# Kernel tuning notes

Hardware: AMD Instinct MI355X
Metric: run time of the kernel (lower is better)

Reference implementation:

```python
import jax, jax.numpy as jnp
import numpy as np

B, S, D, H = 4, 2048, 1024, 16
HD = D // H  # head dim = 64


def setup_inputs() -> dict:
    key = jax.random.key(0)
    ks = jax.random.split(key, 12)
    s = 1.0 / np.sqrt(D)
    return {
        "query": jax.random.normal(ks[0], (B, S, D), jnp.float32),
        "key": jax.random.normal(ks[1], (B, S, D), jnp.float32),
        "value": jax.random.normal(ks[2], (B, S, D), jnp.float32),
        "attention_mask": jnp.zeros((B, S, S), jnp.float32),
        "Wq": jax.random.normal(ks[3], (D, D), jnp.float32) * s,
        "bq": jax.random.normal(ks[4], (D,), jnp.float32) * s,
        "Wk": jax.random.normal(ks[5], (D, D), jnp.float32) * s,
        "bk": jax.random.normal(ks[6], (D,), jnp.float32) * s,
        "Wv": jax.random.normal(ks[7], (D, D), jnp.float32) * s,
        "bv": jax.random.normal(ks[8], (D,), jnp.float32) * s,
        "Wo": jax.random.normal(ks[9], (D, D), jnp.float32) * s,
        "bo": jax.random.normal(ks[10], (D,), jnp.float32) * s,
    }


def reference(query, key, value, attention_mask, Wq, bq, Wk, bk, Wv, bv, Wo, bo):
    # projections (torch Linear: x @ W.T + b)
    q = query @ Wq.T + bq
    k = key @ Wk.T + bk
    v = value @ Wv.T + bv
    # split heads: [B, S, D] -> [B, H, S, HD]
    split = lambda x: x.reshape(B, S, H, HD).transpose(0, 2, 1, 3)
    q, k, v = split(q), split(k), split(v)
    # scores: [B, H, Sq, Sk], scaled and masked (mask broadcast over heads)
    scores = jnp.einsum("bhqd,bhkd->bhqk", q, k) / jnp.sqrt(jnp.asarray(HD, q.dtype))
    scores = scores + attention_mask[:, None, :, :]
    probs = jax.nn.softmax(scores, axis=-1)
    out = jnp.einsum("bhqk,bhkd->bhqd", probs, v)
    # concat heads: [B, H, S, HD] -> [B, S, D]
    out = out.transpose(0, 2, 1, 3).reshape(B, S, D)
    return out @ Wo.T + bo
```

## Files before the change

kernel.cpp:

```cpp
#include <hip/hip_runtime.h>
#include <hip/hip_bf16.h>


typedef float f32x4 __attribute__((ext_vector_type(4)));
typedef float f32x16 __attribute__((ext_vector_type(16)));
typedef short bf16x8 __attribute__((ext_vector_type(8)));

#define LOG2E 1.4426950408889634f

__device__ __forceinline__ void gload_lds16(const void* g, void* l) {
  __builtin_amdgcn_global_load_lds((const __attribute__((address_space(1))) void*)g,
                                   (__attribute__((address_space(3))) void*)l,
                                   16, 0, 0);
}

__device__ __forceinline__ float fast_exp2(float x) {
#if __has_builtin(__builtin_amdgcn_exp2f)
  return __builtin_amdgcn_exp2f(x);
#else
  return exp2f(x);
#endif
}

__device__ __forceinline__ unsigned cvt_pk_bf16(float a, float b) {
  unsigned r;
  asm("v_cvt_pk_bf16_f32 %0, %1, %2" : "=v"(r) : "v"(a), "v"(b));
  return r;
}

__device__ __forceinline__ void pl32swap(unsigned& a, unsigned& b, int hi) {
#if __has_builtin(__builtin_amdgcn_permlane32_swap)
  typedef unsigned uint2v __attribute__((ext_vector_type(2)));
  uint2v r = __builtin_amdgcn_permlane32_swap(a, b, false, false);
  a = r[0];
  b = r[1];
#else
  unsigned ax = __shfl_xor((int)a, 32);
  unsigned bx = __shfl_xor((int)b, 32);
  unsigned na = hi ? bx : a;
  unsigned nb = hi ? b : ax;
  a = na;
  b = nb;
#endif
}

__device__ __forceinline__ bf16x8 lds_read_swz(const __hip_bfloat16* base, int row, int colByte) {
  int off = row * 128 + (colByte ^ ((row & 7) << 4));
  return *(const bf16x8*)((const char*)base + off);
}

__global__ __launch_bounds__(256) void cvt3(const float* __restrict__ s0,
                                            const float* __restrict__ s1,
                                            const float* __restrict__ s2,
                                            __hip_bfloat16* __restrict__ d0,
                                            __hip_bfloat16* __restrict__ d1,
                                            __hip_bfloat16* __restrict__ d2, int n) {
  const float* s = blockIdx.z == 0 ? s0 : (blockIdx.z == 1 ? s1 : s2);
  __hip_bfloat16* d = blockIdx.z == 0 ? d0 : (blockIdx.z == 1 ? d1 : d2);
  int i = (blockIdx.x * 256 + threadIdx.x) * 8;
  if (i + 8 <= n) {
    float4 x = *(const float4*)(s + i);
    float4 y = *(const float4*)(s + i + 4);
    bf16x8 v;
    __hip_bfloat16* hv = (__hip_bfloat16*)&v;
    hv[0] = __float2bfloat16(x.x); hv[1] = __float2bfloat16(x.y);
    hv[2] = __float2bfloat16(x.z); hv[3] = __float2bfloat16(x.w);
    hv[4] = __float2bfloat16(y.x); hv[5] = __float2bfloat16(y.y);
    hv[6] = __float2bfloat16(y.z); hv[7] = __float2bfloat16(y.w);
    *(bf16x8*)(d + i) = v;
  }
}

__global__ __launch_bounds__(256) void cvt4(const float* __restrict__ s0,
                                            const float* __restrict__ s1,
                                            const float* __restrict__ s2,
                                            const float* __restrict__ s3,
                                            __hip_bfloat16* __restrict__ d0,
                                            __hip_bfloat16* __restrict__ d1,
                                            __hip_bfloat16* __restrict__ d2,
                                            __hip_bfloat16* __restrict__ d3, int n) {
  const float* s = blockIdx.z == 0 ? s0 : (blockIdx.z == 1 ? s1 : (blockIdx.z == 2 ? s2 : s3));
  __hip_bfloat16* d = blockIdx.z == 0 ? d0 : (blockIdx.z == 1 ? d1 : (blockIdx.z == 2 ? d2 : d3));
  int i = (blockIdx.x * 256 + threadIdx.x) * 8;
  if (i + 8 <= n) {
    float4 x = *(const float4*)(s + i);
    float4 y = *(const float4*)(s + i + 4);
    bf16x8 v;
    __hip_bfloat16* hv = (__hip_bfloat16*)&v;
    hv[0] = __float2bfloat16(x.x); hv[1] = __float2bfloat16(x.y);
    hv[2] = __float2bfloat16(x.z); hv[3] = __float2bfloat16(x.w);
    hv[4] = __float2bfloat16(y.x); hv[5] = __float2bfloat16(y.y);
    hv[6] = __float2bfloat16(y.z); hv[7] = __float2bfloat16(y.w);
    *(bf16x8*)(d + i) = v;
  }
}

__global__ __launch_bounds__(256) void maskrow(const float* __restrict__ m,
                                               unsigned char* __restrict__ flags) {
  int row = blockIdx.x * 4 + (threadIdx.x >> 6);
  int l = threadIdx.x & 63;
  const float* r = m + (size_t)row * 2048;
  float v0 = r[0];
  bool eq = true;
#pragma unroll
  for (int i = 0; i < 8; i++) {
    float4 x = *(const float4*)(r + l * 4 + i * 256);
    eq &= (x.x == v0) & (x.y == v0) & (x.z == v0) & (x.w == v0);
  }
  unsigned long long b = __ballot((int)eq);
  if (l == 0) flags[row] = (b == ~0ull) ? 1 : 0;
}

__device__ __forceinline__ void gemm_core(const __hip_bfloat16* __restrict__ A,
                                          const __hip_bfloat16* __restrict__ W,
                                          char* smem, int rowbase, int colbase,
                                          f32x4 acc[4][4]) {
  __hip_bfloat16(*As)[64] = (__hip_bfloat16(*)[64])smem;
  __hip_bfloat16(*Bs)[64] = (__hip_bfloat16(*)[64])(smem + 128 * 64 * 2);
  const int t = threadIdx.x;
  const int w = t >> 6, l = t & 63;
  const int wm = w >> 1, wn = w & 1;
  const int lr = l & 15, lg = l >> 4;
  const int srow = l >> 3, schunk = (l & 7) * 8;

#pragma unroll
  for (int m = 0; m < 4; m++)
#pragma unroll
    for (int n = 0; n < 4; n++) acc[m][n] = {0.f, 0.f, 0.f, 0.f};

  for (int kt = 0; kt < 16; ++kt) {
    const int k0 = kt * 64;
#pragma unroll
    for (int i = 0; i < 4; i++) {
      int r = w * 32 + i * 8;
      gload_lds16(A + (size_t)(rowbase + r + srow) * 1024 + k0 + schunk, &As[r][0]);
      gload_lds16(W + (size_t)(colbase + r + srow) * 1024 + k0 + schunk, &Bs[r][0]);
    }
    __syncthreads();
#pragma unroll
    for (int kk = 0; kk < 2; kk++) {
      bf16x8 a[4], b[4];
#pragma unroll
      for (int m = 0; m < 4; m++) a[m] = *(const bf16x8*)&As[wm * 64 + m * 16 + lr][kk * 32 + lg * 8];
#pragma unroll
      for (int n = 0; n < 4; n++) b[n] = *(const bf16x8*)&Bs[wn * 64 + n * 16 + lr][kk * 32 + lg * 8];
#pragma unroll
      for (int m = 0; m < 4; m++)
#pragma unroll
        for (int n = 0; n < 4; n++)
          acc[m][n] = __builtin_amdgcn_mfma_f32_16x16x32_bf16(a[m], b[n], acc[m][n], 0, 0, 0);
    }
    __syncthreads();
  }
}

template <int F32OUT>
__device__ __forceinline__ void gemm_store_rows(f32x4 acc[4][4], const float* __restrict__ bias,
                                                void* __restrict__ out, int rowbase, int colbase,
                                                float scale) {
  const int l = threadIdx.x & 63, w = threadIdx.x >> 6;
  const int wm = w >> 1, wn = w & 1;
  const int lr = l & 15, lg = l >> 4;
#pragma unroll
  for (int m = 0; m < 4; m++)
#pragma unroll
    for (int r = 0; r < 4; r++) {
      int gi = rowbase + wm * 64 + m * 16 + lg * 4 + r;
#pragma unroll
      for (int n = 0; n < 4; n++) {
        int gj = colbase + wn * 64 + n * 16 + lr;
        float v = (acc[m][n][r] + bias[gj]) * scale;
        if (F32OUT)
          ((float*)out)[(size_t)gi * 1024 + gj] = v;
        else
          ((__hip_bfloat16*)out)[(size_t)gi * 1024 + gj] = __float2bfloat16(v);
      }
    }
}

__device__ __forceinline__ void gemm_store_vT(f32x4 acc[4][4], const float* __restrict__ bias,
                                              __hip_bfloat16* __restrict__ out, char* smem,
                                              int rowbase, int colbase) {
  const int t = threadIdx.x, l = t & 63, w = t >> 6;
  const int wm = w >> 1, wn = w & 1;
  const int lr = l & 15, lg = l >> 4;
  __hip_bfloat16* Ts = (__hip_bfloat16*)smem;
#pragma unroll
  for (int m = 0; m < 4; m++)
#pragma unroll
    for (int r = 0; r < 4; r++) {
      int rr = wm * 64 + m * 16 + lg * 4 + r;
#pragma unroll
      for (int n = 0; n < 4; n++) {
        int c = wn * 64 + n * 16 + lr;
        Ts[rr * 130 + c] = __float2bfloat16(acc[m][n][r] + bias[colbase + c]);
      }
    }
  __syncthreads();
  int d = t >> 1, s0 = (t & 1) * 64;
  int gd = colbase + d;
  int h = gd >> 6, hd = gd & 63;
  int gs = rowbase + s0;
  int b = gs >> 11, sl = gs & 2047;
  __hip_bfloat16* dst = out + ((size_t)(b * 16 + h) * 64 + hd) * 2048 + sl;
#pragma unroll
  for (int c8 = 0; c8 < 8; c8++) {
    bf16x8 v;
#pragma unroll
    for (int j = 0; j < 8; j++)
      ((unsigned short*)&v)[j] = ((const unsigned short*)Ts)[(s0 + c8 * 8 + j) * 130 + d];
    *(bf16x8*)(dst + c8 * 8) = v;
  }
}

__global__ __launch_bounds__(256) void gemm_qkv(
    const __hip_bfloat16* __restrict__ vin, const __hip_bfloat16* __restrict__ kin,
    const __hip_bfloat16* __restrict__ qin, const __hip_bfloat16* __restrict__ wv,
    const __hip_bfloat16* __restrict__ wk, const __hip_bfloat16* __restrict__ wq,
    const float* __restrict__ bv, const float* __restrict__ bk, const float* __restrict__ bq,
    __hip_bfloat16* __restrict__ vT, __hip_bfloat16* __restrict__ kp,
    __hip_bfloat16* __restrict__ qp, float qscale) {
  extern __shared__ char smem[];
  const int z = blockIdx.z;
  const __hip_bfloat16* A = z == 0 ? vin : (z == 1 ? kin : qin);
  const __hip_bfloat16* W = z == 0 ? wv : (z == 1 ? wk : wq);
  const float* bias = z == 0 ? bv : (z == 1 ? bk : bq);
  const int rowbase = blockIdx.y * 128;
  const int colbase = blockIdx.x * 128;

  f32x4 acc[4][4];
  gemm_core(A, W, smem, rowbase, colbase, acc);

  if (z == 0) {
    gemm_store_vT(acc, bias, vT, smem, rowbase, colbase);
  } else {
    gemm_store_rows<0>(acc, bias, z == 1 ? (void*)kp : (void*)qp, rowbase, colbase,
                       z == 2 ? qscale : 1.0f);
  }
}

template <int MODE>
__global__ __launch_bounds__(256) void gemm_nt(const __hip_bfloat16* __restrict__ A,
                                               const __hip_bfloat16* __restrict__ W,
                                               const float* __restrict__ bias,
                                               void* __restrict__ out, float scale) {
  extern __shared__ char smem[];
  const int rowbase = blockIdx.y * 128;
  const int colbase = blockIdx.x * 128;
  f32x4 acc[4][4];
  gemm_core(A, W, smem, rowbase, colbase, acc);
  if (MODE == 1)
    gemm_store_vT(acc, bias, (__hip_bfloat16*)out, smem, rowbase, colbase);
  else if (MODE == 0)
    gemm_store_rows<0>(acc, bias, out, rowbase, colbase, scale);
  else
    gemm_store_rows<1>(acc, bias, out, rowbase, colbase, scale);
}

__global__ __launch_bounds__(256, 4) void attn(const __hip_bfloat16* __restrict__ Q,
                                               const __hip_bfloat16* __restrict__ K,
                                               const __hip_bfloat16* __restrict__ Vt,
                                               const float* __restrict__ mask,
                                               const unsigned char* __restrict__ flags,
                                               __hip_bfloat16* __restrict__ O) {
  __shared__ __hip_bfloat16 Ks[2][64][64];
  __shared__ __hip_bfloat16 Vs[2][64][64];

  const int t = threadIdx.x, w = t >> 6, l = t & 63;
  const int l31 = l & 31, hi = l >> 5;
  int lin = blockIdx.y * 16 + blockIdx.x;
  lin = (lin & 7) * 128 + (lin >> 3);
  const int qt = lin & 15, bh = lin >> 4;
  const int b = bh >> 4, h = bh & 15;
  const int q0 = qt * 128 + w * 32;
  const size_t bS = (size_t)b * 2048;
  const int srow = l >> 3;
  const int swchunk = ((l & 7) * 8) ^ (srow << 3);

#define STAGE(dbuf, ktile)                                                             \
  do {                                                                                 \
    int kb_ = (ktile) * 64;                                                            \
    _Pragma("unroll") for (int i_ = 0; i_ < 2; i_++) {                                 \
      int r_ = w * 16 + i_ * 8;                                                        \
      gload_lds16(K + (bS + kb_ + r_ + srow) * 1024 + h * 64 + swchunk,                \
                  &Ks[dbuf][r_][0]);                                                   \
      gload_lds16(Vt + ((size_t)bh * 64 + r_ + srow) * 2048 + kb_ + swchunk,           \
                  &Vs[dbuf][r_][0]);                                                   \
    }                                                                                  \
  } while (0)

  bf16x8 qf[4];
#pragma unroll
  for (int c = 0; c < 4; c++)
    qf[c] = *(const bf16x8*)(Q + (bS + q0 + l31) * 1024 + h * 64 + c * 16 + hi * 8);

  bf16x8 vones;
#pragma unroll
  for (int j = 0; j < 8; j++) ((unsigned short*)&vones)[j] = 0x3F80;

  f32x16 acco[2], psum;
#pragma unroll
  for (int i = 0; i < 16; i++) { acco[0][i] = 0.f; acco[1][i] = 0.f; psum[i] = 0.f; }
  float m2 = -1e30f;

  const bool need_mask = !__all((int)(flags[bS + q0 + l31] != 0));
  const float* mrowf = mask + (bS + q0 + l31) * 2048;

  STAGE(0, 0);
  __syncthreads();
  int cur = 0;

  for (int kt = 0; kt < 32; ++kt) {
    const int kb = kt * 64;
    if (kt < 31) STAGE(cur ^ 1, kt + 1);

    f32x16 sc[2];
    if (need_mask) {
#pragma unroll
      for (int ks = 0; ks < 2; ks++)
#pragma unroll
        for (int g = 0; g < 4; g++) {
          float4 tmp = *(const float4*)(mrowf + kb + ks * 32 + g * 8 + hi * 4);
          sc[ks][g * 4 + 0] = tmp.x * LOG2E; sc[ks][g * 4 + 1] = tmp.y * LOG2E;
          sc[ks][g * 4 + 2] = tmp.z * LOG2E; sc[ks][g * 4 + 3] = tmp.w * LOG2E;
        }
    } else {
#pragma unroll
      for (int i = 0; i < 16; i++) { sc[0][i] = 0.f; sc[1][i] = 0.f; }
    }

    __builtin_amdgcn_s_setprio(1);
#pragma unroll
    for (int c = 0; c < 4; c++) {
      bf16x8 ka0 = lds_read_swz(&Ks[cur][0][0], l31, c * 32 + hi * 16);
      sc[0] = __builtin_amdgcn_mfma_f32_32x32x16_bf16(ka0, qf[c], sc[0], 0, 0, 0);
      bf16x8 ka1 = lds_read_swz(&Ks[cur][0][0], 32 + l31, c * 32 + hi * 16);
      sc[1] = __builtin_amdgcn_mfma_f32_32x32x16_bf16(ka1, qf[c], sc[1], 0, 0, 0);
    }
    __builtin_amdgcn_s_setprio(0);

    float mx[16];
#pragma unroll
    for (int r = 0; r < 16; r++) mx[r] = fmaxf(sc[0][r], sc[1][r]);
#pragma unroll
    for (int s = 8; s >= 1; s >>= 1)
#pragma unroll
      for (int r = 0; r < s; r++) mx[r] = fmaxf(mx[r], mx[r + s]);
    float tmax = fmaxf(mx[0], __shfl_xor(mx[0], 32));

    if (__any(tmax > m2 + 8.0f)) {
      float mn = fmaxf(m2, tmax);
      float rs = fast_exp2(m2 - mn);
      m2 = mn;
#pragma unroll
      for (int r = 0; r < 16; r++) {
        float rsr = __shfl(rs, (r & 3) + 8 * (r >> 2) + 4 * hi);
        psum[r] *= rsr;
        acco[0][r] *= rsr;
        acco[1][r] *= rsr;
      }
    }

    unsigned pk[2][4][2];
#pragma unroll
    for (int ks = 0; ks < 2; ks++)
#pragma unroll
      for (int g = 0; g < 4; g++)
#pragma unroll
        for (int s = 0; s < 2; s++) {
          float p0 = fast_exp2(sc[ks][g * 4 + s * 2] - m2);
          float p1 = fast_exp2(sc[ks][g * 4 + s * 2 + 1] - m2);
          pk[ks][g][s] = cvt_pk_bf16(p0, p1);
        }

    __builtin_amdgcn_s_setprio(1);
#pragma unroll
    for (int ks = 0; ks < 2; ks++) {
#pragma unroll
      for (int c16 = 0; c16 < 2; c16++) {
        unsigned x0 = pk[ks][2 * c16][0], y0 = pk[ks][2 * c16 + 1][0];
        unsigned x1 = pk[ks][2 * c16][1], y1 = pk[ks][2 * c16 + 1][1];
        pl32swap(x0, y0, hi);
        pl32swap(x1, y1, hi);
        bf16x8 pa;
        ((unsigned*)&pa)[0] = x0; ((unsigned*)&pa)[1] = x1;
        ((unsigned*)&pa)[2] = y0; ((unsigned*)&pa)[3] = y1;
        psum = __builtin_amdgcn_mfma_f32_32x32x16_bf16(pa, vones, psum, 0, 0, 0);
#pragma unroll
        for (int ds = 0; ds < 2; ds++) {
          bf16x8 vb = lds_read_swz(&Vs[cur][0][0], ds * 32 + l31, ks * 64 + c16 * 32 + hi * 16);
          acco[ds] = __builtin_amdgcn_mfma_f32_32x32x16_bf16(pa, vb, acco[ds], 0, 0, 0);
        }
      }
    }
    __builtin_amdgcn_s_setprio(0);
    __syncthreads();
    cur ^= 1;
  }
#undef STAGE

#pragma unroll
  for (int r = 0; r < 16; r++) {
    float invr = 1.0f / psum[r];
    int q = q0 + (r & 3) + 8 * (r >> 2) + 4 * hi;
#pragma unroll
    for (int ds = 0; ds < 2; ds++)
      O[(bS + q) * 1024 + h * 64 + ds * 32 + l31] = __float2bfloat16(acco[ds][r] * invr);
  }
}

extern "C" void kernel_launch(void* const* d_in, const int* in_sizes, int n_in,
                              void* d_out, int out_size, void* d_ws, size_t ws_size,
                              hipStream_t stream) {
  const float* q = (const float*)d_in[0];
  const float* k = (const float*)d_in[1];
  const float* v = (const float*)d_in[2];
  const float* msk = (const float*)d_in[3];
  const float* Wq = (const float*)d_in[4];
  const float* bq = (const float*)d_in[5];
  const float* Wk = (const float*)d_in[6];
  const float* bk = (const float*)d_in[7];
  const float* Wv = (const float*)d_in[8];
  const float* bv = (const float*)d_in[9];
  const float* Wo = (const float*)d_in[10];
  const float* bo = (const float*)d_in[11];

  char* ws = (char*)d_ws;
  __hip_bfloat16* qin = (__hip_bfloat16*)(ws);
  __hip_bfloat16* kin = (__hip_bfloat16*)(ws + (16u << 20));
  __hip_bfloat16* vin = (__hip_bfloat16*)(ws + (32u << 20));
  __hip_bfloat16* wqb = (__hip_bfloat16*)(ws + (48u << 20));
  __hip_bfloat16* wkb = (__hip_bfloat16*)(ws + (50u << 20));
  __hip_bfloat16* wvb = (__hip_bfloat16*)(ws + (52u << 20));
  __hip_bfloat16* wob = (__hip_bfloat16*)(ws + (54u << 20));
  __hip_bfloat16* vT  = (__hip_bfloat16*)(ws + (56u << 20));

  const bool merged = ws_size >= (104ull << 20) + 8192;

  dim3 blk(256);
  size_t smem = 33280;
  const float qscale = 0.125f * LOG2E;

  cvt3<<<dim3(4096, 1, 3), blk, 0, stream>>>(q, k, v, qin, kin, vin, 8388608);
  cvt4<<<dim3(512, 1, 4), blk, 0, stream>>>(Wq, Wk, Wv, Wo, wqb, wkb, wvb, wob, 1048576);

  if (merged) {
    __hip_bfloat16* kp = (__hip_bfloat16*)(ws + (72u << 20));
    __hip_bfloat16* qp = (__hip_bfloat16*)(ws + (88u << 20));
    unsigned char* flags = (unsigned char*)(ws + (104u << 20));
    __hip_bfloat16* oat = qin;
    maskrow<<<dim3(2048), blk, 0, stream>>>(msk, flags);
    gemm_qkv<<<dim3(8, 64, 3), blk, smem, stream>>>(vin, kin, qin, wvb, wkb, wqb,
                                                    bv, bk, bq, vT, kp, qp, qscale);
    attn<<<dim3(16, 64), blk, 0, stream>>>(qp, kp, vT, msk, flags, oat);
    gemm_nt<2><<<dim3(8, 64), blk, smem, stream>>>(oat, wob, bo, (float*)d_out, 1.0f);
  } else {
    __hip_bfloat16* kp = vin;
    __hip_bfloat16* qp = kin;
    unsigned char* flags = (unsigned char*)(ws + (72u << 20));
    __hip_bfloat16* oat = qin;
    maskrow<<<dim3(2048), blk, 0, stream>>>(msk, flags);
    gemm_nt<1><<<dim3(8, 64), blk, smem, stream>>>(vin, wvb, bv, vT, 1.0f);
    gemm_nt<0><<<dim3(8, 64), blk, smem, stream>>>(kin, wkb, bk, kp, 1.0f);
    gemm_nt<0><<<dim3(8, 64), blk, smem, stream>>>(qin, wqb, bq, qp, qscale);
    attn<<<dim3(16, 64), blk, 0, stream>>>(qp, kp, vT, msk, flags, oat);
    gemm_nt<2><<<dim3(8, 64), blk, smem, stream>>>(oat, wob, bo, (float*)d_out, 1.0f);
  }
}
```

Measured before the change: 268.4 us.

## Fuse conversion and mask-check kernels; stage GEMM epilogue through LDS for coalesced stores

Merges the three preprocessing launches (activation cast, weight cast, mask-row uniformity check) into one kernel using blockIdx.z to select the work, so two launches and their gaps disappear. The GEMM row-store epilogue now writes accumulators into padded shared memory and then emits wide vector stores per row instead of scattered scalar stores. Shared memory per GEMM block grows slightly to hold the fp32 staging tile, and the fused kernel launches some idle blocks that return early.

```diff
diff --git a/kernel.cpp b/kernel.cpp
--- a/kernel.cpp
+++ b/kernel.cpp
@@ -49,66 +49,53 @@
   return *(const bf16x8*)((const char*)base + off);
 }
 
-__global__ __launch_bounds__(256) void cvt3(const float* __restrict__ s0,
-                                            const float* __restrict__ s1,
-                                            const float* __restrict__ s2,
-                                            __hip_bfloat16* __restrict__ d0,
-                                            __hip_bfloat16* __restrict__ d1,
-                                            __hip_bfloat16* __restrict__ d2, int n) {
-  const float* s = blockIdx.z == 0 ? s0 : (blockIdx.z == 1 ? s1 : s2);
-  __hip_bfloat16* d = blockIdx.z == 0 ? d0 : (blockIdx.z == 1 ? d1 : d2);
-  int i = (blockIdx.x * 256 + threadIdx.x) * 8;
-  if (i + 8 <= n) {
-    float4 x = *(const float4*)(s + i);
-    float4 y = *(const float4*)(s + i + 4);
-    bf16x8 v;
-    __hip_bfloat16* hv = (__hip_bfloat16*)&v;
-    hv[0] = __float2bfloat16(x.x); hv[1] = __float2bfloat16(x.y);
-    hv[2] = __float2bfloat16(x.z); hv[3] = __float2bfloat16(x.w);
-    hv[4] = __float2bfloat16(y.x); hv[5] = __float2bfloat16(y.y);
-    hv[6] = __float2bfloat16(y.z); hv[7] = __float2bfloat16(y.w);
-    *(bf16x8*)(d + i) = v;
-  }
-}
-
-__global__ __launch_bounds__(256) void cvt4(const float* __restrict__ s0,
-                                            const float* __restrict__ s1,
-                                            const float* __restrict__ s2,
-                                            const float* __restrict__ s3,
-                                            __hip_bfloat16* __restrict__ d0,
-                                            __hip_bfloat16* __restrict__ d1,
-                                            __hip_bfloat16* __restrict__ d2,
-                                            __hip_bfloat16* __restrict__ d3, int n) {
-  const float* s = blockIdx.z == 0 ? s0 : (blockIdx.z == 1 ? s1 : (blockIdx.z == 2 ? s2 : s3));
-  __hip_bfloat16* d = blockIdx.z == 0 ? d0 : (blockIdx.z == 1 ? d1 : (blockIdx.z == 2 ? d2 : d3));
-  int i = (blockIdx.x * 256 + threadIdx.x) * 8;
-  if (i + 8 <= n) {
-    float4 x = *(const float4*)(s + i);
-    float4 y = *(const float4*)(s + i + 4);
-    bf16x8 v;
-    __hip_bfloat16* hv = (__hip_bfloat16*)&v;
-    hv[0] = __float2bfloat16(x.x); hv[1] = __float2bfloat16(x.y);
-    hv[2] = __float2bfloat16(x.z); hv[3] = __float2bfloat16(x.w);
-    hv[4] = __float2bfloat16(y.x); hv[5] = __float2bfloat16(y.y);
-    hv[6] = __float2bfloat16(y.z); hv[7] = __float2bfloat16(y.w);
-    *(bf16x8*)(d + i) = v;
-  }
-}
-
-__global__ __launch_bounds__(256) void maskrow(const float* __restrict__ m,
-                                               unsigned char* __restrict__ flags) {
-  int row = blockIdx.x * 4 + (threadIdx.x >> 6);
-  int l = threadIdx.x & 63;
-  const float* r = m + (size_t)row * 2048;
-  float v0 = r[0];
-  bool eq = true;
-#pragma unroll
-  for (int i = 0; i < 8; i++) {
-    float4 x = *(const float4*)(r + l * 4 + i * 256);
-    eq &= (x.x == v0) & (x.y == v0) & (x.z == v0) & (x.w == v0);
-  }
-  unsigned long long b = __ballot((int)eq);
-  if (l == 0) flags[row] = (b == ~0ull) ? 1 : 0;
+__device__ __forceinline__ void cvt8(const float* __restrict__ s, __hip_bfloat16* __restrict__ d) {
+  float4 x = *(const float4*)s;
+  float4 y = *(const float4*)(s + 4);
+  bf16x8 v;
+  __hip_bfloat16* hv = (__hip_bfloat16*)&v;
+  hv[0] = __float2bfloat16(x.x); hv[1] = __float2bfloat16(x.y);
+  hv[2] = __float2bfloat16(x.z); hv[3] = __float2bfloat16(x.w);
+  hv[4] = __float2bfloat16(y.x); hv[5] = __float2bfloat16(y.y);
+  hv[6] = __float2bfloat16(y.z); hv[7] = __float2bfloat16(y.w);
+  *(bf16x8*)d = v;
+}
+
+__global__ __launch_bounds__(256) void cvtall(
+    const float* __restrict__ q, const float* __restrict__ k, const float* __restrict__ v,
+    const float* __restrict__ Wq, const float* __restrict__ Wk,
+    const float* __restrict__ Wv, const float* __restrict__ Wo,
+    const float* __restrict__ msk,
+    __hip_bfloat16* __restrict__ qin, __hip_bfloat16* __restrict__ kin,
+    __hip_bfloat16* __restrict__ vin, __hip_bfloat16* __restrict__ wall,
+    unsigned char* __restrict__ flags) {
+  const int z = blockIdx.z;
+  if (z < 3) {
+    const float* s = z == 0 ? q : (z == 1 ? k : v);
+    __hip_bfloat16* d = z == 0 ? qin : (z == 1 ? kin : vin);
+    int i = (blockIdx.x * 256 + threadIdx.x) * 8;
+    cvt8(s + i, d + i);
+  } else if (z == 3) {
+    if (blockIdx.x >= 2048) return;
+    int i = (blockIdx.x * 256 + threadIdx.x) * 8;
+    int wsel = i >> 20;
+    const float* s = wsel == 0 ? Wq : (wsel == 1 ? Wk : (wsel == 2 ? Wv : Wo));
+    cvt8(s + (i & 1048575), wall + i);
+  } else {
+    if (blockIdx.x >= 2048) return;
+    int row = blockIdx.x * 4 + (threadIdx.x >> 6);
+    int l = threadIdx.x & 63;
+    const float* r = msk + (size_t)row * 2048;
+    float v0 = r[0];
+    bool eq = true;
+#pragma unroll
+    for (int i = 0; i < 8; i++) {
+      float4 x = *(const float4*)(r + l * 4 + i * 256);
+      eq &= (x.x == v0) & (x.y == v0) & (x.z == v0) & (x.w == v0);
+    }
+    unsigned long long b = __ballot((int)eq);
+    if (l == 0) flags[row] = (b == ~0ull) ? 1 : 0;
+  }
 }
 
 __device__ __forceinline__ void gemm_core(const __hip_bfloat16* __restrict__ A,
@@ -156,26 +143,58 @@
 
 template <int F32OUT>
 __device__ __forceinline__ void gemm_store_rows(f32x4 acc[4][4], const float* __restrict__ bias,
-                                                void* __restrict__ out, int rowbase, int colbase,
-                                                float scale) {
-  const int l = threadIdx.x & 63, w = threadIdx.x >> 6;
+                                                void* __restrict__ out, char* smem,
+                                                int rowbase, int colbase, float scale) {
+  const int t = threadIdx.x, l = t & 63, w = t >> 6;
   const int wm = w >> 1, wn = w & 1;
   const int lr = l & 15, lg = l >> 4;
-#pragma unroll
-  for (int m = 0; m < 4; m++)
-#pragma unroll
-    for (int r = 0; r < 4; r++) {
-      int gi = rowbase + wm * 64 + m * 16 + lg * 4 + r;
+  if (F32OUT) {
+    float* Ts = (float*)smem;
+#pragma unroll
+    for (int p = 0; p < 2; p++) {
+      if (wm == p) {
+#pragma unroll
+        for (int m = 0; m < 4; m++)
+#pragma unroll
+          for (int n = 0; n < 4; n++) {
+            float bv_ = bias[colbase + wn * 64 + n * 16 + lr];
+#pragma unroll
+            for (int r = 0; r < 4; r++) {
+              int rl = m * 16 + lg * 4 + r;
+              Ts[rl * 132 + wn * 64 + n * 16 + lr] = (acc[m][n][r] + bv_) * scale;
+            }
+          }
+      }
+      __syncthreads();
+      int row = t >> 2, qd = t & 3;
+      float* dst = (float*)out + (size_t)(rowbase + p * 64 + row) * 1024 + colbase + qd * 32;
+      const float* srcr = Ts + row * 132 + qd * 32;
+#pragma unroll
+      for (int j = 0; j < 8; j++)
+        *(float4*)(dst + j * 4) = *(const float4*)(srcr + j * 4);
+      __syncthreads();
+    }
+  } else {
+    __hip_bfloat16* Ts = (__hip_bfloat16*)smem;
+#pragma unroll
+    for (int m = 0; m < 4; m++)
 #pragma unroll
       for (int n = 0; n < 4; n++) {
-        int gj = colbase + wn * 64 + n * 16 + lr;
-        float v = (acc[m][n][r] + bias[gj]) * scale;
-        if (F32OUT)
-          ((float*)out)[(size_t)gi * 1024 + gj] = v;
-        else
-          ((__hip_bfloat16*)out)[(size_t)gi * 1024 + gj] = __float2bfloat16(v);
+        float bv_ = bias[colbase + wn * 64 + n * 16 + lr];
+#pragma unroll
+        for (int r = 0; r < 4; r++) {
+          int rr = wm * 64 + m * 16 + lg * 4 + r;
+          Ts[rr * 136 + wn * 64 + n * 16 + lr] = __float2bfloat16((acc[m][n][r] + bv_) * scale);
+        }
       }
-    }
+    __syncthreads();
+    int row = t >> 1, hf = t & 1;
+    __hip_bfloat16* dst = (__hip_bfloat16*)out + (size_t)(rowbase + row) * 1024 + colbase + hf * 64;
+    const __hip_bfloat16* srcr = Ts + row * 136 + hf * 64;
+#pragma unroll
+    for (int j = 0; j < 8; j++)
+      *(bf16x8*)(dst + j * 8) = *(const bf16x8*)(srcr + j * 8);
+  }
 }
 
 __device__ __forceinline__ void gemm_store_vT(f32x4 acc[4][4], const float* __restrict__ bias,
@@ -234,7 +253,7 @@
   if (z == 0) {
     gemm_store_vT(acc, bias, vT, smem, rowbase, colbase);
   } else {
-    gemm_store_rows<0>(acc, bias, z == 1 ? (void*)kp : (void*)qp, rowbase, colbase,
+    gemm_store_rows<0>(acc, bias, z == 1 ? (void*)kp : (void*)qp, smem, rowbase, colbase,
                        z == 2 ? qscale : 1.0f);
   }
 }
@@ -252,9 +271,9 @@
   if (MODE == 1)
     gemm_store_vT(acc, bias, (__hip_bfloat16*)out, smem, rowbase, colbase);
   else if (MODE == 0)
-    gemm_store_rows<0>(acc, bias, out, rowbase, colbase, scale);
+    gemm_store_rows<0>(acc, bias, out, smem, rowbase, colbase, scale);
   else
-    gemm_store_rows<1>(acc, bias, out, rowbase, colbase, scale);
+    gemm_store_rows<1>(acc, bias, out, smem, rowbase, colbase, scale);
 }
 
 __global__ __launch_bounds__(256, 4) void attn(const __hip_bfloat16* __restrict__ Q,
@@ -429,27 +448,26 @@
   __hip_bfloat16* qin = (__hip_bfloat16*)(ws);
   __hip_bfloat16* kin = (__hip_bfloat16*)(ws + (16u << 20));
   __hip_bfloat16* vin = (__hip_bfloat16*)(ws + (32u << 20));
-  __hip_bfloat16* wqb = (__hip_bfloat16*)(ws + (48u << 20));
-  __hip_bfloat16* wkb = (__hip_bfloat16*)(ws + (50u << 20));
-  __hip_bfloat16* wvb = (__hip_bfloat16*)(ws + (52u << 20));
-  __hip_bfloat16* wob = (__hip_bfloat16*)(ws + (54u << 20));
+  __hip_bfloat16* wall = (__hip_bfloat16*)(ws + (48u << 20));
+  __hip_bfloat16* wqb = wall;
+  __hip_bfloat16* wkb = wall + (1u << 20);
+  __hip_bfloat16* wvb = wall + (2u << 20);
+  __hip_bfloat16* wob = wall + (3u << 20);
   __hip_bfloat16* vT  = (__hip_bfloat16*)(ws + (56u << 20));
 
   const bool merged = ws_size >= (104ull << 20) + 8192;
 
   dim3 blk(256);
-  size_t smem = 33280;
+  size_t smem = 34816;
   const float qscale = 0.125f * LOG2E;
-
-  cvt3<<<dim3(4096, 1, 3), blk, 0, stream>>>(q, k, v, qin, kin, vin, 8388608);
-  cvt4<<<dim3(512, 1, 4), blk, 0, stream>>>(Wq, Wk, Wv, Wo, wqb, wkb, wvb, wob, 1048576);
 
   if (merged) {
     __hip_bfloat16* kp = (__hip_bfloat16*)(ws + (72u << 20));
     __hip_bfloat16* qp = (__hip_bfloat16*)(ws + (88u << 20));
     unsigned char* flags = (unsigned char*)(ws + (104u << 20));
     __hip_bfloat16* oat = qin;
-    maskrow<<<dim3(2048), blk, 0, stream>>>(msk, flags);
+    cvtall<<<dim3(4096, 1, 5), blk, 0, stream>>>(q, k, v, Wq, Wk, Wv, Wo, msk,
+                                                 qin, kin, vin, wall, flags);
     gemm_qkv<<<dim3(8, 64, 3), blk, smem, stream>>>(vin, kin, qin, wvb, wkb, wqb,
                                                     bv, bk, bq, vT, kp, qp, qscale);
     attn<<<dim3(16, 64), blk, 0, stream>>>(qp, kp, vT, msk, flags, oat);
@@ -459,7 +477,8 @@
     __hip_bfloat16* qp = kin;
     unsigned char* flags = (unsigned char*)(ws + (72u << 20));
     __hip_bfloat16* oat = qin;
-    maskrow<<<dim3(2048), blk, 0, stream>>>(msk, flags);
+    cvtall<<<dim3(4096, 1, 5), blk, 0, stream>>>(q, k, v, Wq, Wk, Wv, Wo, msk,
+                                                 qin, kin, vin, wall, flags);
     gemm_nt<1><<<dim3(8, 64), blk, smem, stream>>>(vin, wvb, bv, vT, 1.0f);
     gemm_nt<0><<<dim3(8, 64), blk, smem, stream>>>(kin, wkb, bk, kp, 1.0f);
     gemm_nt<0><<<dim3(8, 64), blk, smem, stream>>>(qin, wqb, bq, qp, qscale);
```

Measured after the change: 283.0 us. 1.05x slower.
